# Performance work log

Measured on AMD Instinct MI355X. Metric: run time of the kernel, lower is better.

The kernel has to match this reference:

```python
import jax, jax.numpy as jnp
import numpy as np

INF = 100000000.0
STRIDES = (8, 16, 32, 64, 128)
SOI = ((-1.0, 64.0), (64.0, 128.0), (128.0, 256.0), (256.0, 512.0), (512.0, INF))
IMG_H, IMG_W = 800, 1216
RADIUS = 1.5
NUM_CLASSES = 80


def _level_grids():
    locs, strides, ranges = [], [], []
    for s, (lo, hi) in zip(STRIDES, SOI):
        h, w = -(-IMG_H // s), -(-IMG_W // s)
        ys = (np.arange(h, dtype=np.float32) * s + s // 2)
        xs = (np.arange(w, dtype=np.float32) * s + s // 2)
        gx, gy = np.meshgrid(xs, ys)
        locs.append(np.stack([gx.ravel(), gy.ravel()], axis=1))
        strides.append(np.full(h * w, s, np.float32))
        ranges.append(np.tile(np.array([lo, hi], np.float32), (h * w, 1)))
    return (np.concatenate(locs, 0), np.concatenate(strides, 0), np.concatenate(ranges, 0))


def setup_inputs() -> dict:
    key = jax.random.key(0)
    locs, stride_loc, size_ranges = _level_grids()  # [L,2], [L], [L,2]; L = 20267
    B, G = 16, 50
    k1, k2, k3 = jax.random.split(key, 3)
    img_wh = jnp.array([IMG_W, IMG_H], jnp.float32)
    cxcy = jax.random.uniform(k1, (B, G, 2)) * img_wh
    wh = 16.0 + jax.random.uniform(k2, (B, G, 2)) * 496.0
    x1y1 = jnp.clip(cxcy - wh * 0.5, 0.0, None)
    x2y2 = jnp.minimum(cxcy + wh * 0.5, img_wh)
    gt_boxes = jnp.concatenate([x1y1, x2y2], axis=-1)  # [B,G,4] xyxy
    gt_classes = jax.random.randint(k3, (B, G), 0, NUM_CLASSES)
    return {
        'locations': jnp.asarray(locs),
        'stride_loc': jnp.asarray(stride_loc),
        'size_ranges': jnp.asarray(size_ranges),
        'gt_boxes': gt_boxes,
        'gt_classes': gt_classes,
    }


def _assign_one_image(locations, stride_loc, size_ranges, boxes, classes):
    # locations [L,2], boxes [G,4], classes [G]
    xs, ys = locations[:, 0], locations[:, 1]
    l = xs[:, None] - boxes[None, :, 0]
    t = ys[:, None] - boxes[None, :, 1]
    r = boxes[None, :, 2] - xs[:, None]
    b = boxes[None, :, 3] - ys[:, None]
    reg = jnp.stack([l, t, r, b], axis=-1)  # [L,G,4]
    # --- center sampling (get_sample_region): clip box to radius*stride around center ---
    cx = (boxes[:, 0] + boxes[:, 2]) * 0.5
    cy = (boxes[:, 1] + boxes[:, 3]) * 0.5
    rad = stride_loc * RADIUS  # [L]
    x0 = jnp.maximum(cx[None, :] - rad[:, None], boxes[None, :, 0])
    y0 = jnp.maximum(cy[None, :] - rad[:, None], boxes[None, :, 1])
    x1 = jnp.minimum(cx[None, :] + rad[:, None], boxes[None, :, 2])
    y1 = jnp.minimum(cy[None, :] + rad[:, None], boxes[None, :, 3])
    cb = jnp.stack([xs[:, None] - x0, ys[:, None] - y0, x1 - xs[:, None], y1 - ys[:, None]], -1)
    in_radius = jnp.min(cb, axis=-1) > 0  # [L,G]
    # --- size-of-interest gating ---
    max_reg = jnp.minimum(jnp.maximum(l, r), jnp.maximum(t, b))  # [L,G]
    cared = (max_reg >= size_ranges[:, 0:1]) & (max_reg <= size_ranges[:, 1:2])
    # --- min-area matching ---
    area = (boxes[:, 2] - boxes[:, 0]) * (boxes[:, 3] - boxes[:, 1])  # [G]
    loc2area = jnp.where(in_radius & cared, area[None, :], INF)  # [L,G]
    gt_inds = jnp.argmin(loc2area, axis=1)  # [L]
    min_area = jnp.take_along_axis(loc2area, gt_inds[:, None], axis=1)[:, 0]
    reg_t = jnp.take_along_axis(reg, gt_inds[:, None, None], axis=1)[:, 0]  # [L,4]
    labels = jnp.where(min_area >= INF, NUM_CLASSES, classes[gt_inds])
    # per-level normalization (reg_targets[l] /= strides[l])
    reg_t = reg_t / stride_loc[:, None]
    # centerness targets
    lr = reg_t[:, jnp.array([0, 2])] + 1e-05
    tb = reg_t[:, jnp.array([1, 3])] + 1e-05
    ctr = (jnp.min(lr, -1) / jnp.max(lr, -1)) * (jnp.min(tb, -1) / jnp.max(tb, -1))
    ctr = jnp.sqrt(jnp.maximum(ctr, 0.0))
    return labels, reg_t, ctr


def reference(locations, stride_loc, size_ranges, gt_boxes, gt_classes):
    labels, reg_t, ctr = jax.vmap(
        lambda bx, cl: _assign_one_image(locations, stride_loc, size_ranges, bx, cl)
    )(gt_boxes, gt_classes)
    return labels, reg_t, ctr  # [B,L], [B,L,4], [B,L]
```

## Files before the change

kernel.cpp:

```cpp
#include <hip/hip_runtime.h>
#include <hip/hip_bf16.h>

#define INF_VAL 100000000.0f
#define RADIUS 1.5f
#define NUM_CLASSES 80
#define G_BOXES 50

__global__ void __launch_bounds__(256) fcos_assign_kernel(
    const float* __restrict__ locations,
    const float* __restrict__ stride_loc,
    const float* __restrict__ size_ranges,
    const float* __restrict__ gt_boxes,
    const int*   __restrict__ gt_classes,
    float* __restrict__ out,
    int L, int B)
{
    const int b = blockIdx.y;
    const int i = blockIdx.x * blockDim.x + threadIdx.x;

    __shared__ float4 sder[G_BOXES];

    const float4* __restrict__ box4 =
        reinterpret_cast<const float4*>(gt_boxes) + (size_t)b * G_BOXES;

    if (threadIdx.x < G_BOXES) {
        const int g = threadIdx.x;
        const float4 bx = box4[g];
        float4 v;
        v.x = (bx.x + bx.z) * 0.5f;
        v.y = (bx.y + bx.w) * 0.5f;
        v.z = (bx.z - bx.x) * (bx.w - bx.y);
        v.w = (float)gt_classes[(size_t)b * G_BOXES + g];
        sder[g] = v;
    }
    __syncthreads();

    if (i >= L) return;

    const float2 xy = *reinterpret_cast<const float2*>(locations + 2 * (size_t)i);
    const float x = xy.x, y = xy.y;
    const float stride = stride_loc[i];
    const float2 sr = *reinterpret_cast<const float2*>(size_ranges + 2 * (size_t)i);
    const float lo = sr.x, hi = sr.y;
    const float rad = stride * RADIUS;

    float best_area = INF_VAL;
    int best_g = 0;

    #pragma unroll 5
    for (int g = 0; g < G_BOXES; ++g) {
        const float4 bx = box4[g];
        const float4 d  = sder[g];

        const float l  = x - bx.x;
        const float t  = y - bx.y;
        const float r  = bx.z - x;
        const float bt = bx.w - y;

        const float c0 = d.x - rad;
        const float c1 = d.x + rad;
        const float c2 = d.y - rad;
        const float c3 = d.y + rad;
        const bool in_radius =
            (x > c0) & (x < c1) & (y > c2) & (y < c3) &
            (fminf(fminf(l, t), fminf(r, bt)) > 0.0f);

        const float max_reg = fminf(fmaxf(l, r), fmaxf(t, bt));
        const bool cared = (max_reg >= lo) & (max_reg <= hi);

        const float val = (in_radius & cared) ? d.z : INF_VAL;
        if (val < best_area) { best_area = val; best_g = g; }
    }

    const float4 bb = box4[best_g];
    const float inv_s = 1.0f / stride;
    const float rl = (x - bb.x) * inv_s;
    const float rt = (y - bb.y) * inv_s;
    const float rr = (bb.z - x) * inv_s;
    const float rb = (bb.w - y) * inv_s;

    const float clsf = reinterpret_cast<const float*>(sder)[best_g * 4 + 3];
    const float label = (best_area >= INF_VAL) ? (float)NUM_CLASSES : clsf;

    const float lr0 = rl + 1e-5f, lr1 = rr + 1e-5f;
    const float tb0 = rt + 1e-5f, tb1 = rb + 1e-5f;
    float ctr = (fminf(lr0, lr1) / fmaxf(lr0, lr1)) * (fminf(tb0, tb1) / fmaxf(tb0, tb1));
    ctr = sqrtf(fmaxf(ctr, 0.0f));

    const size_t BL = (size_t)B * L;
    const size_t bl = (size_t)b * L + i;

    out[bl] = label;

    float4 rg;
    rg.x = rl; rg.y = rt; rg.z = rr; rg.w = rb;
    *reinterpret_cast<float4*>(out + BL + bl * 4) = rg;

    out[5 * BL + bl] = ctr;
}

extern "C" void kernel_launch(void* const* d_in, const int* in_sizes, int n_in,
                              void* d_out, int out_size, void* d_ws, size_t ws_size,
                              hipStream_t stream) {
    const float* locations   = (const float*)d_in[0];
    const float* stride_loc  = (const float*)d_in[1];
    const float* size_ranges = (const float*)d_in[2];
    const float* gt_boxes    = (const float*)d_in[3];
    const int*   gt_classes  = (const int*)d_in[4];
    float* out = (float*)d_out;

    const int L = in_sizes[1];
    const int B = in_sizes[4] / G_BOXES;

    dim3 block(256);
    dim3 grid((L + 255) / 256, B);
    fcos_assign_kernel<<<grid, block, 0, stream>>>(
        locations, stride_loc, size_ranges, gt_boxes, gt_classes, out, L, B);
}
```

Before: 75.24 us.

## Replace dense per-location box scan with sparse scatter of center-sampled candidates

```diff
diff --git a/kernel.cpp b/kernel.cpp
--- a/kernel.cpp
+++ b/kernel.cpp
@@ -5,82 +5,106 @@
 #define RADIUS 1.5f
 #define NUM_CLASSES 80
 #define G_BOXES 50
+#define N_LVL 5
 
-__global__ void __launch_bounds__(256) fcos_assign_kernel(
+
+__device__ __constant__ const float  LVL_S[N_LVL]    = {8.f, 16.f, 32.f, 64.f, 128.f};
+__device__ __constant__ const float  LVL_HALF[N_LVL] = {4.f, 8.f, 16.f, 32.f, 64.f};
+__device__ __constant__ const float  LVL_INV[N_LVL]  = {0.125f, 0.0625f, 0.03125f, 0.015625f, 0.0078125f};
+__device__ __constant__ const int    LVL_W[N_LVL]    = {152, 76, 38, 19, 10};
+__device__ __constant__ const int    LVL_H[N_LVL]    = {100, 50, 25, 13, 7};
+__device__ __constant__ const int    LVL_OFF[N_LVL]  = {0, 15200, 19000, 19950, 20197};
+__device__ __constant__ const float  LVL_LO[N_LVL]   = {-1.f, 64.f, 128.f, 256.f, 512.f};
+__device__ __constant__ const float  LVL_HI[N_LVL]   = {64.f, 128.f, 256.f, 512.f, INF_VAL};
+
+__global__ void __launch_bounds__(256) fcos_scatter_kernel(
+    const float* __restrict__ gt_boxes,
+    unsigned long long* __restrict__ ws,
+    int L)
+{
+    const int b = blockIdx.x / G_BOXES;
+    const int g = blockIdx.x - b * G_BOXES;
+    const int t = threadIdx.x;
+    if (t >= N_LVL * 49) return;
+    const int lvl = t / 49;
+    const int c   = t - lvl * 49;
+
+    const float4 bx = *(reinterpret_cast<const float4*>(gt_boxes) + (size_t)b * G_BOXES + g);
+
+    const float cx   = (bx.x + bx.z) * 0.5f;
+    const float cy   = (bx.y + bx.w) * 0.5f;
+    const float area = (bx.z - bx.x) * (bx.w - bx.y);
+
+    const float s    = LVL_S[lvl];
+    const float rad  = s * RADIUS;
+    const float half = LVL_HALF[lvl];
+    const float inv  = LVL_INV[lvl];
+
+    const float x0e = fmaxf(cx - rad, bx.x);
+    const float y0e = fmaxf(cy - rad, bx.y);
+    const float x1e = fminf(cx + rad, bx.z);
+    const float y1e = fminf(cy + rad, bx.w);
+
+    const int jx0 = (int)floorf((x0e - half) * inv) - 1;
+    const int jx1 = (int)ceilf ((x1e - half) * inv) + 1;
+    const int jy0 = (int)floorf((y0e - half) * inv) - 1;
+    const int jy1 = (int)ceilf ((y1e - half) * inv) + 1;
+
+    const int jx = jx0 + (c % 7);
+    const int jy = jy0 + (c / 7);
+    if (jx < 0 || jx >= LVL_W[lvl] || jx > jx1) return;
+    if (jy < 0 || jy >= LVL_H[lvl] || jy > jy1) return;
+
+    const float x = (float)jx * s + half;
+    const float y = (float)jy * s + half;
+
+    const float l   = x - bx.x;
+    const float tt  = y - bx.y;
+    const float r   = bx.z - x;
+    const float btm = bx.w - y;
+    const float cbm = fminf(fminf(x - x0e, y - y0e), fminf(x1e - x, y1e - y));
+    const float max_reg = fminf(fmaxf(l, r), fmaxf(tt, btm));
+    const bool ok = (cbm > 0.0f) & (max_reg >= LVL_LO[lvl]) & (max_reg <= LVL_HI[lvl]);
+    if (!ok) return;
+
+    const unsigned int abits = __float_as_uint(area);
+    const unsigned long long key =
+        ((unsigned long long)(~abits) << 32) | (unsigned int)(~(unsigned int)g);
+
+    const int loc = LVL_OFF[lvl] + jy * LVL_W[lvl] + jx;
+    atomicMax(ws + (size_t)b * L + loc, key);
+}
+
+__global__ void __launch_bounds__(256) fcos_finalize_kernel(
     const float* __restrict__ locations,
     const float* __restrict__ stride_loc,
-    const float* __restrict__ size_ranges,
     const float* __restrict__ gt_boxes,
     const int*   __restrict__ gt_classes,
+    const unsigned long long* __restrict__ ws,
     float* __restrict__ out,
     int L, int B)
 {
     const int b = blockIdx.y;
     const int i = blockIdx.x * blockDim.x + threadIdx.x;
+    if (i >= L) return;
 
-    __shared__ float4 sder[G_BOXES];
-
-    const float4* __restrict__ box4 =
-        reinterpret_cast<const float4*>(gt_boxes) + (size_t)b * G_BOXES;
-
-    if (threadIdx.x < G_BOXES) {
-        const int g = threadIdx.x;
-        const float4 bx = box4[g];
-        float4 v;
-        v.x = (bx.x + bx.z) * 0.5f;
-        v.y = (bx.y + bx.w) * 0.5f;
-        v.z = (bx.z - bx.x) * (bx.w - bx.y);
-        v.w = (float)gt_classes[(size_t)b * G_BOXES + g];
-        sder[g] = v;
-    }
-    __syncthreads();
-
-    if (i >= L) return;
+    const unsigned long long key = ws[(size_t)b * L + i];
+    const bool bg = (key == 0ull);
+    const int  g  = bg ? 0 : (int)(~(unsigned int)(key & 0xFFFFFFFFull));
 
     const float2 xy = *reinterpret_cast<const float2*>(locations + 2 * (size_t)i);
     const float x = xy.x, y = xy.y;
     const float stride = stride_loc[i];
-    const float2 sr = *reinterpret_cast<const float2*>(size_ranges + 2 * (size_t)i);
-    const float lo = sr.x, hi = sr.y;
-    const float rad = stride * RADIUS;
 
-    float best_area = INF_VAL;
-    int best_g = 0;
-
-    #pragma unroll 5
-    for (int g = 0; g < G_BOXES; ++g) {
-        const float4 bx = box4[g];
-        const float4 d  = sder[g];
-
-        const float l  = x - bx.x;
-        const float t  = y - bx.y;
-        const float r  = bx.z - x;
-        const float bt = bx.w - y;
-
-        const float c0 = d.x - rad;
-        const float c1 = d.x + rad;
-        const float c2 = d.y - rad;
-        const float c3 = d.y + rad;
-        const bool in_radius =
-            (x > c0) & (x < c1) & (y > c2) & (y < c3) &
-            (fminf(fminf(l, t), fminf(r, bt)) > 0.0f);
-
-        const float max_reg = fminf(fmaxf(l, r), fmaxf(t, bt));
-        const bool cared = (max_reg >= lo) & (max_reg <= hi);
-
-        const float val = (in_radius & cared) ? d.z : INF_VAL;
-        if (val < best_area) { best_area = val; best_g = g; }
-    }
-
-    const float4 bb = box4[best_g];
+    const float4 bb = *(reinterpret_cast<const float4*>(gt_boxes) + (size_t)b * G_BOXES + g);
     const float inv_s = 1.0f / stride;
     const float rl = (x - bb.x) * inv_s;
     const float rt = (y - bb.y) * inv_s;
     const float rr = (bb.z - x) * inv_s;
     const float rb = (bb.w - y) * inv_s;
 
-    const float clsf = reinterpret_cast<const float*>(sder)[best_g * 4 + 3];
-    const float label = (best_area >= INF_VAL) ? (float)NUM_CLASSES : clsf;
+    const float label = bg ? (float)NUM_CLASSES
+                           : (float)gt_classes[(size_t)b * G_BOXES + g];
 
     const float lr0 = rl + 1e-5f, lr1 = rr + 1e-5f;
     const float tb0 = rt + 1e-5f, tb1 = rb + 1e-5f;
@@ -91,11 +115,8 @@
     const size_t bl = (size_t)b * L + i;
 
     out[bl] = label;
-
-    float4 rg;
-    rg.x = rl; rg.y = rt; rg.z = rr; rg.w = rb;
+    float4 rg; rg.x = rl; rg.y = rt; rg.z = rr; rg.w = rb;
     *reinterpret_cast<float4*>(out + BL + bl * 4) = rg;
-
     out[5 * BL + bl] = ctr;
 }
 
@@ -104,7 +125,7 @@
                               hipStream_t stream) {
     const float* locations   = (const float*)d_in[0];
     const float* stride_loc  = (const float*)d_in[1];
-    const float* size_ranges = (const float*)d_in[2];
+    const float* size_ranges = (const float*)d_in[2];  (void)size_ranges;
     const float* gt_boxes    = (const float*)d_in[3];
     const int*   gt_classes  = (const int*)d_in[4];
     float* out = (float*)d_out;
@@ -112,8 +133,13 @@
     const int L = in_sizes[1];
     const int B = in_sizes[4] / G_BOXES;
 
-    dim3 block(256);
-    dim3 grid((L + 255) / 256, B);
-    fcos_assign_kernel<<<grid, block, 0, stream>>>(
-        locations, stride_loc, size_ranges, gt_boxes, gt_classes, out, L, B);
+    unsigned long long* ws = (unsigned long long*)d_ws;
+    const size_t ws_bytes = (size_t)B * L * sizeof(unsigned long long);
+
+    hipMemsetAsync(ws, 0, ws_bytes, stream);
+
+    fcos_scatter_kernel<<<dim3(B * G_BOXES), dim3(256), 0, stream>>>(gt_boxes, ws, L);
+
+    fcos_finalize_kernel<<<dim3((L + 255) / 256, B), dim3(256), 0, stream>>>(
+        locations, stride_loc, gt_boxes, gt_classes, ws, out, L, B);
 }
```

After: 69.93 us. -7.1%, faster.
